# Performance work log

Measured on AMD Instinct MI355X. Metric: run time of the kernel, lower is better.

Reference implementation:

```python
import jax, jax.numpy as jnp
import numpy as np

# dims
B, P, A, ATTR = 64, 32, 1, 7          # batch, num_predictors, num_anchors, bbox_attrib
C = A * P * ATTR                       # 224 channels
R = 4096                               # row_size (angular cells)
N_LAB = 32                             # labels per image
CELL_ANGLE, CELL_DEPTH = 0.1, 1.0
ANCHORS = jnp.array([1.6, 3.9], jnp.float32)
LXY, LWL, LROT, LOBJ, LNOOBJ = 10.0, 10.0, 20.0, 20.0, 1.0


def setup_inputs() -> dict:
    key = jax.random.key(0)
    k1, k2, k3, k4, k5 = jax.random.split(key, 5)
    preds = jax.random.normal(k1, (B, C, R), jnp.float32)
    # labels: (angle, depth, w, l, rot_a, rot_b, conf); conf>=0 => has_labels True
    ang = jax.random.uniform(k2, (B, N_LAB, 1), minval=-R * CELL_ANGLE / 2, maxval=R * CELL_ANGLE / 2)
    dep = jax.random.uniform(k3, (B, N_LAB, 1), minval=0.0, maxval=P * CELL_DEPTH)
    wl = jax.random.uniform(k4, (B, N_LAB, 2), minval=0.5, maxval=4.0)
    rot = jax.random.uniform(k5, (B, N_LAB, 2), minval=-1.0, maxval=1.0)
    conf = jnp.ones((B, N_LAB, 1), jnp.float32)
    labels = jnp.concatenate([ang, dep, wl, rot, conf], axis=-1)
    return {"preds": preds, "labels": labels}


def _safe_log(x):
    # torch BCE clamps log at -100
    return jnp.maximum(jnp.log(x), -100.0)


def _per_image(pred, lab):
    # pred: [C, R] -> [R, P, A*7]  (view + permute + view in the torch code)
    p = pred.T.reshape(R, P, A * ATTR)
    xy = jax.nn.sigmoid(p[..., :2])
    wl = p[..., 2:4]
    rot = jnp.tanh(p[..., 4:6])
    conf = jax.nn.sigmoid(p[..., 6])

    # data-dependent cell assignment
    ang = lab[:, 0] + R * CELL_ANGLE / 2
    i = jnp.clip(jnp.floor(ang / CELL_ANGLE).astype(jnp.int32), 0, R - 1)
    j = jnp.clip(jnp.floor(lab[:, 1] / CELL_DEPTH).astype(jnp.int32), 0, P - 1)
    new_lab = jnp.concatenate(
        [
            (ang / CELL_ANGLE - i.astype(ang.dtype))[:, None],
            (lab[:, 1] / CELL_DEPTH - j.astype(ang.dtype))[:, None],
            lab[:, 2:6],
            jnp.ones((N_LAB, 1), lab.dtype),
        ],
        axis=-1,
    )
    tgt = jnp.zeros((R, P, ATTR), pred.dtype).at[i, j].set(new_lab)   # scatter targets
    obj = jnp.zeros((R, P), pred.dtype).at[i, j].set(1.0)             # obj mask

    tgt_wl = jnp.log(tgt[..., 2:4] / ANCHORS + 1e-16)
    m = obj[..., None]
    l_xy = jnp.sum(m * (xy - tgt[..., :2]) ** 2)
    l_wl = jnp.sum(m * (wl - tgt_wl) ** 2)
    l_rot = jnp.sum(m * (rot - tgt[..., 4:6]) ** 2)

    t = tgt[..., 6]
    bce = -(t * _safe_log(conf) + (1.0 - t) * _safe_log(1.0 - conf))
    l_obj = jnp.sum(obj * bce)
    l_noobj = jnp.sum((1.0 - obj) * bce)
    return jnp.stack([l_xy, l_wl, l_rot, l_obj, l_noobj])


def reference(preds, labels):
    losses = jnp.sum(jax.vmap(_per_image)(preds, labels), axis=0)
    l_xy, l_wl, l_rot, l_obj, l_noobj = losses
    total = LXY * l_xy + LWL * l_wl + LROT * l_rot + LOBJ * l_obj + LNOOBJ * l_noobj
    return (total, l_xy, l_wl, l_rot, l_obj, l_noobj)
```

## Files before the change

kernel.cpp:

```cpp
#include <hip/hip_runtime.h>
#include <math.h>

#define BB   64
#define PP   32
#define RR   4096
#define NATT 7
#define NLAB 32
#define NCH  (PP * NATT)


__device__ __forceinline__ float sigmoidf_(float x) {
    return 1.0f / (1.0f + expf(-x));
}

__global__ __launch_bounds__(256) void noobj_kernel(const float* __restrict__ preds,
                                                    float* __restrict__ acc) {
    const float4* p4 = reinterpret_cast<const float4*>(preds);
    const int total4 = BB * PP * RR / 4;
    float local = 0.0f;
    for (int f = blockIdx.x * blockDim.x + threadIdx.x; f < total4;
         f += gridDim.x * blockDim.x) {
        int row = f >> 10;
        int b   = row >> 5;
        int pp  = row & 31;
        int a4  = ((b * NCH + pp * NATT + 6) << 10) + (f & 1023);
        float4 v = p4[a4];
        float xs[4] = {v.x, v.y, v.z, v.w};
#pragma unroll
        for (int u = 0; u < 4; ++u) {
            float conf = sigmoidf_(xs[u]);
            float l    = fmaxf(logf(1.0f - conf), -100.0f);
            local -= l;
        }
    }
#pragma unroll
    for (int off = 32; off > 0; off >>= 1) local += __shfl_down(local, off);
    __shared__ float s[4];
    int lane = threadIdx.x & 63, w = threadIdx.x >> 6;
    if (lane == 0) s[w] = local;
    __syncthreads();
    if (threadIdx.x == 0) {
        atomicAdd(&acc[4], s[0] + s[1] + s[2] + s[3]);
    }
}

__global__ __launch_bounds__(256) void label_kernel(const float* __restrict__ preds,
                                                    const float* __restrict__ labels,
                                                    float* __restrict__ acc) {
    int idx = blockIdx.x * blockDim.x + threadIdx.x;
    if (idx >= BB * NLAB) return;
    int b = idx >> 5;
    int k = idx & 31;
    const float* lab = labels + (size_t)(b * NLAB + k) * NATT;

    float ang = lab[0] + 204.8f;
    float af  = ang / 0.1f;
    int i = (int)floorf(af);
    i = min(max(i, 0), RR - 1);
    float dep = lab[1];
    int j = (int)floorf(dep);
    j = min(max(j, 0), PP - 1);

    for (int kk = k + 1; kk < NLAB; ++kk) {
        const float* l2 = labels + (size_t)(b * NLAB + kk) * NATT;
        float a2 = (l2[0] + 204.8f) / 0.1f;
        int i2 = min(max((int)floorf(a2), 0), RR - 1);
        int j2 = min(max((int)floorf(l2[1]), 0), PP - 1);
        if (i2 == i && j2 == j) return;
    }

    float fx = af  - (float)i;
    float fy = dep - (float)j;

    const float* pb = preds + ((size_t)b * NCH + (size_t)j * NATT) * RR + i;
    float p0 = pb[0 * RR], p1 = pb[1 * RR], p2 = pb[2 * RR], p3 = pb[3 * RR];
    float p4 = pb[4 * RR], p5 = pb[5 * RR], p6 = pb[6 * RR];

    float s0 = sigmoidf_(p0), s1 = sigmoidf_(p1);
    float l_xy = (s0 - fx) * (s0 - fx) + (s1 - fy) * (s1 - fy);

    float tw = logf(lab[2] / 1.6f + 1e-16f);
    float tl = logf(lab[3] / 3.9f + 1e-16f);
    float l_wl = (p2 - tw) * (p2 - tw) + (p3 - tl) * (p3 - tl);

    float r0 = tanhf(p4), r1 = tanhf(p5);
    float l_rot = (r0 - lab[4]) * (r0 - lab[4]) + (r1 - lab[5]) * (r1 - lab[5]);

    float conf  = sigmoidf_(p6);
    float l_obj = -fmaxf(logf(conf), -100.0f);
    float noobj_part = -fmaxf(logf(1.0f - conf), -100.0f);

    atomicAdd(&acc[0], l_xy);
    atomicAdd(&acc[1], l_wl);
    atomicAdd(&acc[2], l_rot);
    atomicAdd(&acc[3], l_obj);
    atomicAdd(&acc[4], -noobj_part);
}

__global__ void finalize_kernel(const float* __restrict__ acc, float* __restrict__ out) {
    if (threadIdx.x == 0 && blockIdx.x == 0) {
        float xy = acc[0], wl = acc[1], rot = acc[2], obj = acc[3], noobj = acc[4];
        out[0] = 10.0f * xy + 10.0f * wl + 20.0f * rot + 20.0f * obj + 1.0f * noobj;
        out[1] = xy;
        out[2] = wl;
        out[3] = rot;
        out[4] = obj;
        out[5] = noobj;
    }
}

extern "C" void kernel_launch(void* const* d_in, const int* in_sizes, int n_in,
                              void* d_out, int out_size, void* d_ws, size_t ws_size,
                              hipStream_t stream) {
    const float* preds  = (const float*)d_in[0];
    const float* labels = (const float*)d_in[1];
    float* out = (float*)d_out;
    float* acc = (float*)d_ws;

    hipMemsetAsync(acc, 0, 8 * sizeof(float), stream);

    label_kernel<<<(BB * NLAB + 255) / 256, 256, 0, stream>>>(preds, labels, acc);
    noobj_kernel<<<2048, 256, 0, stream>>>(preds, acc);
    finalize_kernel<<<1, 64, 0, stream>>>(acc, out);
}
```

Before: 317.1 us.

## Fuse label and noobj kernels, replace atomics with per-block partials reduction

Merges the label-cell loss computation into the streaming noobj kernel so a single launch handles both, with the first 2048 threads also processing labels. Global atomics and the memset are replaced by per-block partial sums written to workspace and a separate deterministic reduction kernel. This removes a kernel launch, the memset and atomic contention, at the cost of a small tail of extra work on the early blocks and a second pass over the partials.

New measurement: 287.0 us. 9.5% less time.

```diff
diff --git a/kernel.cpp b/kernel.cpp
--- a/kernel.cpp
+++ b/kernel.cpp
@@ -1,25 +1,29 @@
 #include <hip/hip_runtime.h>
 #include <math.h>
 
-#define BB   64
-#define PP   32
-#define RR   4096
-#define NATT 7
-#define NLAB 32
-#define NCH  (PP * NATT)
+#define BB    64
+#define PP    32
+#define RR    4096
+#define NATT  7
+#define NLAB  32
+#define NCH   (PP * NATT)
+#define GRID1 2048
+#define BLK1  256
+#define TOT4  (BB * PP * RR / 4)
 
 
 __device__ __forceinline__ float sigmoidf_(float x) {
     return 1.0f / (1.0f + expf(-x));
 }
 
-__global__ __launch_bounds__(256) void noobj_kernel(const float* __restrict__ preds,
-                                                    float* __restrict__ acc) {
+__global__ __launch_bounds__(BLK1) void fused_kernel(const float* __restrict__ preds,
+                                                     const float* __restrict__ labels,
+                                                     float* __restrict__ partials) {
+    const int gid = blockIdx.x * BLK1 + threadIdx.x;
+    float l_xy = 0.0f, l_wl = 0.0f, l_rot = 0.0f, l_obj = 0.0f, l_noobj = 0.0f;
+
     const float4* p4 = reinterpret_cast<const float4*>(preds);
-    const int total4 = BB * PP * RR / 4;
-    float local = 0.0f;
-    for (int f = blockIdx.x * blockDim.x + threadIdx.x; f < total4;
-         f += gridDim.x * blockDim.x) {
+    for (int f = gid; f < TOT4; f += GRID1 * BLK1) {
         int row = f >> 10;
         int b   = row >> 5;
         int pp  = row & 31;
@@ -29,78 +33,90 @@
 #pragma unroll
         for (int u = 0; u < 4; ++u) {
             float conf = sigmoidf_(xs[u]);
-            float l    = fmaxf(logf(1.0f - conf), -100.0f);
-            local -= l;
+            l_noobj -= fmaxf(logf(1.0f - conf), -100.0f);
         }
     }
+
+    if (gid < BB * NLAB) {
+        int b = gid >> 5;
+        int k = gid & 31;
+        const float* lab = labels + (size_t)(b * NLAB + k) * NATT;
+
+        float af = (lab[0] + 204.8f) / 0.1f;
+        int i = min(max((int)floorf(af), 0), RR - 1);
+        float dep = lab[1];
+        int j = min(max((int)floorf(dep), 0), PP - 1);
+
+        bool overwritten = false;
+        for (int kk = k + 1; kk < NLAB; ++kk) {
+            const float* l2 = labels + (size_t)(b * NLAB + kk) * NATT;
+            float a2 = (l2[0] + 204.8f) / 0.1f;
+            int i2 = min(max((int)floorf(a2), 0), RR - 1);
+            int j2 = min(max((int)floorf(l2[1]), 0), PP - 1);
+            if (i2 == i && j2 == j) { overwritten = true; break; }
+        }
+
+        if (!overwritten) {
+            float fx = af  - (float)i;
+            float fy = dep - (float)j;
+
+            const float* pb = preds + ((size_t)b * NCH + (size_t)j * NATT) * RR + i;
+            float p0 = pb[0 * RR], p1 = pb[1 * RR], p2 = pb[2 * RR], p3 = pb[3 * RR];
+            float q0 = pb[4 * RR], q1 = pb[5 * RR], p6 = pb[6 * RR];
+
+            float s0 = sigmoidf_(p0), s1 = sigmoidf_(p1);
+            l_xy = (s0 - fx) * (s0 - fx) + (s1 - fy) * (s1 - fy);
+
+            float tw = logf(lab[2] / 1.6f + 1e-16f);
+            float tl = logf(lab[3] / 3.9f + 1e-16f);
+            l_wl = (p2 - tw) * (p2 - tw) + (p3 - tl) * (p3 - tl);
+
+            float r0 = tanhf(q0), r1 = tanhf(q1);
+            l_rot = (r0 - lab[4]) * (r0 - lab[4]) + (r1 - lab[5]) * (r1 - lab[5]);
+
+            float conf = sigmoidf_(p6);
+            l_obj = -fmaxf(logf(conf), -100.0f);
+            l_noobj += fmaxf(logf(1.0f - conf), -100.0f);
+        }
+    }
+
+    float v0 = l_xy, v1 = l_wl, v2 = l_rot, v3 = l_obj, v4 = l_noobj;
 #pragma unroll
-    for (int off = 32; off > 0; off >>= 1) local += __shfl_down(local, off);
-    __shared__ float s[4];
+    for (int off = 32; off > 0; off >>= 1) {
+        v0 += __shfl_down(v0, off);
+        v1 += __shfl_down(v1, off);
+        v2 += __shfl_down(v2, off);
+        v3 += __shfl_down(v3, off);
+        v4 += __shfl_down(v4, off);
+    }
+    __shared__ float s[4][5];
     int lane = threadIdx.x & 63, w = threadIdx.x >> 6;
-    if (lane == 0) s[w] = local;
+    if (lane == 0) {
+        s[w][0] = v0; s[w][1] = v1; s[w][2] = v2; s[w][3] = v3; s[w][4] = v4;
+    }
     __syncthreads();
     if (threadIdx.x == 0) {
-        atomicAdd(&acc[4], s[0] + s[1] + s[2] + s[3]);
+        float* dst = partials + (size_t)blockIdx.x * 5;
+#pragma unroll
+        for (int c = 0; c < 5; ++c)
+            dst[c] = s[0][c] + s[1][c] + s[2][c] + s[3][c];
     }
 }
 
-__global__ __launch_bounds__(256) void label_kernel(const float* __restrict__ preds,
-                                                    const float* __restrict__ labels,
-                                                    float* __restrict__ acc) {
-    int idx = blockIdx.x * blockDim.x + threadIdx.x;
-    if (idx >= BB * NLAB) return;
-    int b = idx >> 5;
-    int k = idx & 31;
-    const float* lab = labels + (size_t)(b * NLAB + k) * NATT;
-
-    float ang = lab[0] + 204.8f;
-    float af  = ang / 0.1f;
-    int i = (int)floorf(af);
-    i = min(max(i, 0), RR - 1);
-    float dep = lab[1];
-    int j = (int)floorf(dep);
-    j = min(max(j, 0), PP - 1);
-
-    for (int kk = k + 1; kk < NLAB; ++kk) {
-        const float* l2 = labels + (size_t)(b * NLAB + kk) * NATT;
-        float a2 = (l2[0] + 204.8f) / 0.1f;
-        int i2 = min(max((int)floorf(a2), 0), RR - 1);
-        int j2 = min(max((int)floorf(l2[1]), 0), PP - 1);
-        if (i2 == i && j2 == j) return;
-    }
-
-    float fx = af  - (float)i;
-    float fy = dep - (float)j;
-
-    const float* pb = preds + ((size_t)b * NCH + (size_t)j * NATT) * RR + i;
-    float p0 = pb[0 * RR], p1 = pb[1 * RR], p2 = pb[2 * RR], p3 = pb[3 * RR];
-    float p4 = pb[4 * RR], p5 = pb[5 * RR], p6 = pb[6 * RR];
-
-    float s0 = sigmoidf_(p0), s1 = sigmoidf_(p1);
-    float l_xy = (s0 - fx) * (s0 - fx) + (s1 - fy) * (s1 - fy);
-
-    float tw = logf(lab[2] / 1.6f + 1e-16f);
-    float tl = logf(lab[3] / 3.9f + 1e-16f);
-    float l_wl = (p2 - tw) * (p2 - tw) + (p3 - tl) * (p3 - tl);
-
-    float r0 = tanhf(p4), r1 = tanhf(p5);
-    float l_rot = (r0 - lab[4]) * (r0 - lab[4]) + (r1 - lab[5]) * (r1 - lab[5]);
-
-    float conf  = sigmoidf_(p6);
-    float l_obj = -fmaxf(logf(conf), -100.0f);
-    float noobj_part = -fmaxf(logf(1.0f - conf), -100.0f);
-
-    atomicAdd(&acc[0], l_xy);
-    atomicAdd(&acc[1], l_wl);
-    atomicAdd(&acc[2], l_rot);
-    atomicAdd(&acc[3], l_obj);
-    atomicAdd(&acc[4], -noobj_part);
-}
-
-__global__ void finalize_kernel(const float* __restrict__ acc, float* __restrict__ out) {
-    if (threadIdx.x == 0 && blockIdx.x == 0) {
-        float xy = acc[0], wl = acc[1], rot = acc[2], obj = acc[3], noobj = acc[4];
-        out[0] = 10.0f * xy + 10.0f * wl + 20.0f * rot + 20.0f * obj + 1.0f * noobj;
+__global__ __launch_bounds__(320) void reduce_kernel(const float* __restrict__ partials,
+                                                     float* __restrict__ out) {
+    int w    = threadIdx.x >> 6;
+    int lane = threadIdx.x & 63;
+    float sum = 0.0f;
+    for (int b = lane; b < GRID1; b += 64) sum += partials[(size_t)b * 5 + w];
+#pragma unroll
+    for (int off = 32; off > 0; off >>= 1) sum += __shfl_down(sum, off);
+    __shared__ float comp[5];
+    if (lane == 0) comp[w] = sum;
+    __syncthreads();
+    if (threadIdx.x == 0) {
+        float xy = comp[0], wl = comp[1], rot = comp[2], obj = comp[3], noobj = comp[4];
+        out[0] = 10.0f * xy + 10.0f * wl + 20.0f * rot + 20.0f * obj + noobj;
         out[1] = xy;
         out[2] = wl;
         out[3] = rot;
@@ -114,12 +130,9 @@
                               hipStream_t stream) {
     const float* preds  = (const float*)d_in[0];
     const float* labels = (const float*)d_in[1];
-    float* out = (float*)d_out;
-    float* acc = (float*)d_ws;
+    float* out      = (float*)d_out;
+    float* partials = (float*)d_ws;
 
-    hipMemsetAsync(acc, 0, 8 * sizeof(float), stream);
-
-    label_kernel<<<(BB * NLAB + 255) / 256, 256, 0, stream>>>(preds, labels, acc);
-    noobj_kernel<<<2048, 256, 0, stream>>>(preds, acc);
-    finalize_kernel<<<1, 64, 0, stream>>>(acc, out);
+    fused_kernel<<<GRID1, BLK1, 0, stream>>>(preds, labels, partials);
+    reduce_kernel<<<1, 320, 0, stream>>>(partials, out);
 }
```
